# Optimization experiments

Measured on AMD Instinct MI355X. Metric: run time of the kernel, lower is better.

## Reference

```python
import jax, jax.numpy as jnp
import numpy as np

B, S, T = 4096, 2048, 2  # batch of conversations, turns per conversation, num_tags


def setup_inputs() -> dict:
    key = jax.random.key(0)
    k1, k2, k3, k4, k5, k6 = jax.random.split(key, 6)
    emissions = jax.random.normal(k1, (B, S, T), dtype=jnp.float32)
    # learned transition matrices for DistanceCRF branch order:
    # [even2odd, I0, D_consecutive, D_nonconsecutive]
    trans_params = jax.random.normal(k2, (4, T, T), dtype=jnp.float32) * 0.1
    tags = jax.random.randint(k3, (B, S), 0, T)
    who2who = jax.random.randint(k4, (B, S), 0, 2)
    intime = jax.random.randint(k5, (B, S), 0, 3)
    distance = jax.random.randint(k6, (B, S), 0, 4)
    return {"emissions": emissions, "trans_params": trans_params, "tags": tags,
            "who2who": who2who, "intime": intime, "distance": distance}


def _select_trans(trans_params, who2who, intime, distance):
    """Per-step transition matrix selection (DistanceCRF logic).
    Returns [B, S, T, T]."""
    Tn = trans_params.shape[-1]
    # index 0 = zero 'padding' matrix (who2who == -1 case)
    bank = jnp.concatenate([jnp.zeros((1, Tn, Tn), trans_params.dtype), trans_params], axis=0)
    sel = jnp.where(who2who == -1, 0,
          jnp.where(who2who == 1, 1,          # even2odd
          jnp.where(intime == 0, 2,           # I0
          jnp.where(distance == 0, 3, 4))))   # D_consecutive / D_nonconsecutive
    return bank[sel]


def reference(emissions, trans_params, tags, who2who, intime, distance):
    Bn, Sn, Tn = emissions.shape
    trans = _select_trans(trans_params, who2who, intime, distance)  # [B,S,T,T]

    # ---- gold path score ----
    em_gold = jnp.take_along_axis(emissions, tags[..., None], axis=-1)[..., 0].sum(-1)  # [B]
    oh_prev = jax.nn.one_hot(tags[:, :-1], Tn, dtype=emissions.dtype)  # [B,S-1,T]
    oh_cur = jax.nn.one_hot(tags[:, 1:], Tn, dtype=emissions.dtype)
    tr_gold = jnp.einsum('bsij,bsi,bsj->b', trans[:, 1:], oh_prev, oh_cur)  # [B]
    gold_score = em_gold + tr_gold

    # ---- log partition via forward recursion (note: transition added at t=0 too,
    # matching the original implementation) ----
    def step(alpha, xs):
        em_t, tr_t = xs  # [B,T], [B,T,T]
        new_alpha = jax.nn.logsumexp(alpha[:, :, None] + em_t[:, None, :] + tr_t, axis=1)
        return new_alpha, None

    alpha0 = jnp.zeros((Bn, Tn), emissions.dtype)
    xs = (jnp.swapaxes(emissions, 0, 1), jnp.swapaxes(trans, 0, 1))  # [S,B,T], [S,B,T,T]
    alpha, _ = jax.lax.scan(step, alpha0, xs)
    total_score = jax.nn.logsumexp(alpha, axis=-1)  # [B]

    return jnp.stack([gold_score, total_score])  # [2, B]
```

## Files before the change

kernel.cpp:

```cpp
#include <hip/hip_runtime.h>
#include <math.h>

#define Bn 4096
#define Sn 2048
#define BLOCK 256
#define CHUNK (Sn / BLOCK)

__global__ __launch_bounds__(BLOCK, 2) void crf_fwd(
    const float* __restrict__ emissions,
    const float* __restrict__ trans_params,
    const int*   __restrict__ tags,
    const int*   __restrict__ who2who,
    const int*   __restrict__ intime,
    const int*   __restrict__ distance,
    float*       __restrict__ out)
{
    const int b  = blockIdx.x;
    const int t  = threadIdx.x;
    const long base = (long)b * Sn;
    const int s0 = t * CHUNK;

    __shared__ __align__(16) float lbank[20];
    __shared__ __align__(16) float ebank[20];
    __shared__ float wm[4][6];

    const int4* tp = (const int4*)(tags     + base) + t * 2;
    const int4* wp = (const int4*)(who2who  + base) + t * 2;
    const int4* ip = (const int4*)(intime   + base) + t * 2;
    const int4* dp = (const int4*)(distance + base) + t * 2;
    const float4* ep = (const float4*)(emissions + base * 2) + t * 4;

    float4 e0 = ep[0], e1 = ep[1], e2 = ep[2], e3 = ep[3];
    int4 ta = tp[0], tb = tp[1];
    int4 wa = wp[0], wb = wp[1];
    int4 ia = ip[0], ib = ip[1];
    int4 da = dp[0], db = dp[1];
    int prev_tag = (t > 0) ? tags[base + s0 - 1] : 0;

    if (t < 20) {
        float v = (t < 4) ? 0.0f : trans_params[t - 4];
        lbank[t] = v;
        ebank[t] = __expf(v);
    }
    __syncthreads();

    int wv[CHUNK]   = {wa.x, wa.y, wa.z, wa.w, wb.x, wb.y, wb.z, wb.w};
    int iv[CHUNK]   = {ia.x, ia.y, ia.z, ia.w, ib.x, ib.y, ib.z, ib.w};
    int dv[CHUNK]   = {da.x, da.y, da.z, da.w, db.x, db.y, db.z, db.w};
    int tagv[CHUNK] = {ta.x, ta.y, ta.z, ta.w, tb.x, tb.y, tb.z, tb.w};
    float emv[CHUNK][2] = {
        {e0.x, e0.y}, {e0.z, e0.w}, {e1.x, e1.y}, {e1.z, e1.w},
        {e2.x, e2.y}, {e2.z, e2.w}, {e3.x, e3.y}, {e3.z, e3.w}};

    int sel[CHUNK];
    #pragma unroll
    for (int k = 0; k < CHUNK; ++k) {
        int w = wv[k], it = iv[k], d = dv[k];
        sel[k] = (w == -1) ? 0 : (w == 1) ? 1 : (it == 0) ? 2 : (d == 0) ? 3 : 4;
    }
    float4 P[CHUNK];
    #pragma unroll
    for (int k = 0; k < CHUNK; ++k)
        P[k] = *(const float4*)(ebank + sel[k] * 4);

    float x[CHUNK][2];
    #pragma unroll
    for (int k = 0; k < CHUNK; ++k) {
        x[k][0] = __expf(emv[k][0]);
        x[k][1] = __expf(emv[k][1]);
    }

    float m00 = P[0].x * x[0][0], m01 = P[0].y * x[0][1];
    float m10 = P[0].z * x[0][0], m11 = P[0].w * x[0][1];
    float gold = 0.0f;

    #pragma unroll
    for (int k = 1; k < CHUNK; ++k) {
        float n00 = fmaf(m00, P[k].x, m01 * P[k].z) * x[k][0];
        float n01 = fmaf(m00, P[k].y, m01 * P[k].w) * x[k][1];
        float n10 = fmaf(m10, P[k].x, m11 * P[k].z) * x[k][0];
        float n11 = fmaf(m10, P[k].y, m11 * P[k].w) * x[k][1];
        m00 = n00; m01 = n01; m10 = n10; m11 = n11;
    }

    #pragma unroll
    for (int k = 0; k < CHUNK; ++k) {
        int tg = tagv[k];
        gold += tg ? emv[k][1] : emv[k][0];
        if (k > 0 || t > 0) {
            int pt = (k == 0) ? prev_tag : tagv[k - 1];
            gold += lbank[(sel[k] << 2) + (pt << 1) + tg];
        }
    }

    float mx  = fmaxf(fmaxf(m00, m01), fmaxf(m10, m11));
    float inv = 1.0f / mx;
    float L   = __logf(mx);
    m00 *= inv; m01 *= inv; m10 *= inv; m11 *= inv;

    #pragma unroll
    for (int m = 1; m < 64; m <<= 1) {
        float o00 = __shfl_xor(m00, m);
        float o01 = __shfl_xor(m01, m);
        float o10 = __shfl_xor(m10, m);
        float o11 = __shfl_xor(m11, m);
        float oL  = __shfl_xor(L, m);
        float og  = __shfl_xor(gold, m);
        bool up = (t & m) != 0;
        float a00 = up ? o00 : m00, a01 = up ? o01 : m01;
        float a10 = up ? o10 : m10, a11 = up ? o11 : m11;
        float b00 = up ? m00 : o00, b01 = up ? m01 : o01;
        float b10 = up ? m10 : o10, b11 = up ? m11 : o11;
        m00 = fmaf(a00, b00, a01 * b10);
        m01 = fmaf(a00, b01, a01 * b11);
        m10 = fmaf(a10, b00, a11 * b10);
        m11 = fmaf(a10, b01, a11 * b11);
        L += oL;
        gold += og;
    }

    int wave = t >> 6;
    if ((t & 63) == 0) {
        wm[wave][0] = m00; wm[wave][1] = m01;
        wm[wave][2] = m10; wm[wave][3] = m11;
        wm[wave][4] = L;   wm[wave][5] = gold;
    }
    __syncthreads();

    if (t == 0) {
        float r00 = wm[0][0], r01 = wm[0][1], r10 = wm[0][2], r11 = wm[0][3];
        float Ls = wm[0][4], g = wm[0][5];
        #pragma unroll
        for (int q = 1; q < 4; ++q) {
            float q00 = wm[q][0], q01 = wm[q][1], q10 = wm[q][2], q11 = wm[q][3];
            float n00 = fmaf(r00, q00, r01 * q10);
            float n01 = fmaf(r00, q01, r01 * q11);
            float n10 = fmaf(r10, q00, r11 * q10);
            float n11 = fmaf(r10, q01, r11 * q11);
            r00 = n00; r01 = n01; r10 = n10; r11 = n11;
            Ls += wm[q][4];
            g  += wm[q][5];
        }
        float tot = Ls + __logf(r00 + r01 + r10 + r11);
        out[b]      = g;
        out[Bn + b] = tot;
    }
}

extern "C" void kernel_launch(void* const* d_in, const int* in_sizes, int n_in,
                              void* d_out, int out_size, void* d_ws, size_t ws_size,
                              hipStream_t stream) {
    const float* emissions    = (const float*)d_in[0];
    const float* trans_params = (const float*)d_in[1];
    const int*   tags         = (const int*)d_in[2];
    const int*   who2who      = (const int*)d_in[3];
    const int*   intime       = (const int*)d_in[4];
    const int*   distance     = (const int*)d_in[5];
    float* out = (float*)d_out;

    crf_fwd<<<dim3(Bn), dim3(BLOCK), 0, stream>>>(
        emissions, trans_params, tags, who2who, intime, distance, out);
}
```

Measured before the change: 200.8 us.

## Split CRF forward into chunk kernel and per-wave reduction kernel

Splits the fused kernel in two. The first kernel computes per-thread chunk matrices and writes them, normalized, to workspace. A second kernel reduces each sequence with one wave, doing a serial fold of 4 chunks per lane and then a shuffle tree that renormalizes at every step, so the block-wide shared-memory barrier and single-thread tail go away. The change also computes exp and loads transitions inside the recurrence loop instead of precomputing arrays, which should lower register pressure. The cost is an extra launch plus a workspace round trip of about 24 MB, and extra log and reciprocal work in the tree.

```diff
diff --git a/kernel.cpp b/kernel.cpp
--- a/kernel.cpp
+++ b/kernel.cpp
@@ -5,42 +5,44 @@
 #define Sn 2048
 #define BLOCK 256
 #define CHUNK (Sn / BLOCK)
+#define NM (Bn * BLOCK)
 
-__global__ __launch_bounds__(BLOCK, 2) void crf_fwd(
+__global__ __launch_bounds__(BLOCK) void crf_chunk(
     const float* __restrict__ emissions,
     const float* __restrict__ trans_params,
     const int*   __restrict__ tags,
     const int*   __restrict__ who2who,
     const int*   __restrict__ intime,
     const int*   __restrict__ distance,
-    float*       __restrict__ out)
+    float2*      __restrict__ wsA,
+    float2*      __restrict__ wsB,
+    float2*      __restrict__ wsC)
 {
-    const int b  = blockIdx.x;
-    const int t  = threadIdx.x;
+    const int b = blockIdx.x;
+    const int c = threadIdx.x;
     const long base = (long)b * Sn;
-    const int s0 = t * CHUNK;
+    const int s0 = c * CHUNK;
 
     __shared__ __align__(16) float lbank[20];
     __shared__ __align__(16) float ebank[20];
-    __shared__ float wm[4][6];
 
-    const int4* tp = (const int4*)(tags     + base) + t * 2;
-    const int4* wp = (const int4*)(who2who  + base) + t * 2;
-    const int4* ip = (const int4*)(intime   + base) + t * 2;
-    const int4* dp = (const int4*)(distance + base) + t * 2;
-    const float4* ep = (const float4*)(emissions + base * 2) + t * 4;
+    const int4* tp = (const int4*)(tags     + base) + c * 2;
+    const int4* wp = (const int4*)(who2who  + base) + c * 2;
+    const int4* ip = (const int4*)(intime   + base) + c * 2;
+    const int4* dp = (const int4*)(distance + base) + c * 2;
+    const float4* ep = (const float4*)(emissions + base * 2) + c * 4;
 
     float4 e0 = ep[0], e1 = ep[1], e2 = ep[2], e3 = ep[3];
     int4 ta = tp[0], tb = tp[1];
     int4 wa = wp[0], wb = wp[1];
     int4 ia = ip[0], ib = ip[1];
     int4 da = dp[0], db = dp[1];
-    int prev_tag = (t > 0) ? tags[base + s0 - 1] : 0;
+    int prev_tag = (c > 0) ? tags[base + s0 - 1] : 0;
 
-    if (t < 20) {
-        float v = (t < 4) ? 0.0f : trans_params[t - 4];
-        lbank[t] = v;
-        ebank[t] = __expf(v);
+    if (c < 20) {
+        float v = (c < 4) ? 0.0f : trans_params[c - 4];
+        lbank[c] = v;
+        ebank[c] = __expf(v);
     }
     __syncthreads();
 
@@ -58,36 +60,27 @@
         int w = wv[k], it = iv[k], d = dv[k];
         sel[k] = (w == -1) ? 0 : (w == 1) ? 1 : (it == 0) ? 2 : (d == 0) ? 3 : 4;
     }
-    float4 P[CHUNK];
-    #pragma unroll
-    for (int k = 0; k < CHUNK; ++k)
-        P[k] = *(const float4*)(ebank + sel[k] * 4);
 
-    float x[CHUNK][2];
-    #pragma unroll
-    for (int k = 0; k < CHUNK; ++k) {
-        x[k][0] = __expf(emv[k][0]);
-        x[k][1] = __expf(emv[k][1]);
-    }
-
-    float m00 = P[0].x * x[0][0], m01 = P[0].y * x[0][1];
-    float m10 = P[0].z * x[0][0], m11 = P[0].w * x[0][1];
-    float gold = 0.0f;
-
+    float4 P0 = *(const float4*)(ebank + sel[0] * 4);
+    float m00 = P0.x * __expf(emv[0][0]), m01 = P0.y * __expf(emv[0][1]);
+    float m10 = P0.z * __expf(emv[0][0]), m11 = P0.w * __expf(emv[0][1]);
     #pragma unroll
     for (int k = 1; k < CHUNK; ++k) {
-        float n00 = fmaf(m00, P[k].x, m01 * P[k].z) * x[k][0];
-        float n01 = fmaf(m00, P[k].y, m01 * P[k].w) * x[k][1];
-        float n10 = fmaf(m10, P[k].x, m11 * P[k].z) * x[k][0];
-        float n11 = fmaf(m10, P[k].y, m11 * P[k].w) * x[k][1];
+        float4 P = *(const float4*)(ebank + sel[k] * 4);
+        float x0 = __expf(emv[k][0]), x1 = __expf(emv[k][1]);
+        float n00 = fmaf(m00, P.x, m01 * P.z) * x0;
+        float n01 = fmaf(m00, P.y, m01 * P.w) * x1;
+        float n10 = fmaf(m10, P.x, m11 * P.z) * x0;
+        float n11 = fmaf(m10, P.y, m11 * P.w) * x1;
         m00 = n00; m01 = n01; m10 = n10; m11 = n11;
     }
 
+    float gold = 0.0f;
     #pragma unroll
     for (int k = 0; k < CHUNK; ++k) {
         int tg = tagv[k];
         gold += tg ? emv[k][1] : emv[k][0];
-        if (k > 0 || t > 0) {
+        if (k > 0 || c > 0) {
             int pt = (k == 0) ? prev_tag : tagv[k - 1];
             gold += lbank[(sel[k] << 2) + (pt << 1) + tg];
         }
@@ -96,7 +89,54 @@
     float mx  = fmaxf(fmaxf(m00, m01), fmaxf(m10, m11));
     float inv = 1.0f / mx;
     float L   = __logf(mx);
-    m00 *= inv; m01 *= inv; m10 *= inv; m11 *= inv;
+
+    const int gid = b * BLOCK + c;
+    wsA[gid] = make_float2(m00 * inv, m01 * inv);
+    wsB[gid] = make_float2(m10 * inv, m11 * inv);
+    wsC[gid] = make_float2(L, gold);
+}
+
+__global__ __launch_bounds__(BLOCK) void crf_reduce(
+    const float2* __restrict__ wsA,
+    const float2* __restrict__ wsB,
+    const float2* __restrict__ wsC,
+    float*        __restrict__ out)
+{
+    const int lane = threadIdx.x & 63;
+    const int wave = threadIdx.x >> 6;
+    const int b = blockIdx.x * 4 + wave;
+
+    const int idx4 = b * (BLOCK / 2) + lane * 2;
+    const float4* A4 = (const float4*)wsA;
+    const float4* B4 = (const float4*)wsB;
+    const float4* C4 = (const float4*)wsC;
+    float4 a0 = A4[idx4], a1 = A4[idx4 + 1];
+    float4 b0 = B4[idx4], b1 = B4[idx4 + 1];
+    float4 c0 = C4[idx4], c1 = C4[idx4 + 1];
+
+    float m00 = a0.x, m01 = a0.y, m10 = b0.x, m11 = b0.y;
+    float L = c0.x, gold = c0.y;
+    {
+        float q00[3] = {a0.z, a1.x, a1.z};
+        float q01[3] = {a0.w, a1.y, a1.w};
+        float q10[3] = {b0.z, b1.x, b1.z};
+        float q11[3] = {b0.w, b1.y, b1.w};
+        float qL[3]  = {c0.z, c1.x, c1.z};
+        float qg[3]  = {c0.w, c1.y, c1.w};
+        #pragma unroll
+        for (int q = 0; q < 3; ++q) {
+            float n00 = fmaf(m00, q00[q], m01 * q10[q]);
+            float n01 = fmaf(m00, q01[q], m01 * q11[q]);
+            float n10 = fmaf(m10, q00[q], m11 * q10[q]);
+            float n11 = fmaf(m10, q01[q], m11 * q11[q]);
+            m00 = n00; m01 = n01; m10 = n10; m11 = n11;
+            L += qL[q]; gold += qg[q];
+        }
+        float mx  = fmaxf(fmaxf(m00, m01), fmaxf(m10, m11));
+        float inv = 1.0f / mx;
+        L += __logf(mx);
+        m00 *= inv; m01 *= inv; m10 *= inv; m11 *= inv;
+    }
 
     #pragma unroll
     for (int m = 1; m < 64; m <<= 1) {
@@ -106,43 +146,26 @@
         float o11 = __shfl_xor(m11, m);
         float oL  = __shfl_xor(L, m);
         float og  = __shfl_xor(gold, m);
-        bool up = (t & m) != 0;
-        float a00 = up ? o00 : m00, a01 = up ? o01 : m01;
-        float a10 = up ? o10 : m10, a11 = up ? o11 : m11;
-        float b00 = up ? m00 : o00, b01 = up ? m01 : o01;
-        float b10 = up ? m10 : o10, b11 = up ? m11 : o11;
-        m00 = fmaf(a00, b00, a01 * b10);
-        m01 = fmaf(a00, b01, a01 * b11);
-        m10 = fmaf(a10, b00, a11 * b10);
-        m11 = fmaf(a10, b01, a11 * b11);
+        bool up = (lane & m) != 0;
+        float x00 = up ? o00 : m00, x01 = up ? o01 : m01;
+        float x10 = up ? o10 : m10, x11 = up ? o11 : m11;
+        float y00 = up ? m00 : o00, y01 = up ? m01 : o01;
+        float y10 = up ? m10 : o10, y11 = up ? m11 : o11;
+        m00 = fmaf(x00, y00, x01 * y10);
+        m01 = fmaf(x00, y01, x01 * y11);
+        m10 = fmaf(x10, y00, x11 * y10);
+        m11 = fmaf(x10, y01, x11 * y11);
         L += oL;
         gold += og;
+        float mx  = fmaxf(fmaxf(m00, m01), fmaxf(m10, m11));
+        float inv = 1.0f / mx;
+        L += __logf(mx);
+        m00 *= inv; m01 *= inv; m10 *= inv; m11 *= inv;
     }
 
-    int wave = t >> 6;
-    if ((t & 63) == 0) {
-        wm[wave][0] = m00; wm[wave][1] = m01;
-        wm[wave][2] = m10; wm[wave][3] = m11;
-        wm[wave][4] = L;   wm[wave][5] = gold;
-    }
-    __syncthreads();
-
-    if (t == 0) {
-        float r00 = wm[0][0], r01 = wm[0][1], r10 = wm[0][2], r11 = wm[0][3];
-        float Ls = wm[0][4], g = wm[0][5];
-        #pragma unroll
-        for (int q = 1; q < 4; ++q) {
-            float q00 = wm[q][0], q01 = wm[q][1], q10 = wm[q][2], q11 = wm[q][3];
-            float n00 = fmaf(r00, q00, r01 * q10);
-            float n01 = fmaf(r00, q01, r01 * q11);
-            float n10 = fmaf(r10, q00, r11 * q10);
-            float n11 = fmaf(r10, q01, r11 * q11);
-            r00 = n00; r01 = n01; r10 = n10; r11 = n11;
-            Ls += wm[q][4];
-            g  += wm[q][5];
-        }
-        float tot = Ls + __logf(r00 + r01 + r10 + r11);
-        out[b]      = g;
+    if (lane == 0) {
+        float tot = L + __logf(m00 + m01 + m10 + m11);
+        out[b]      = gold;
         out[Bn + b] = tot;
     }
 }
@@ -158,6 +181,13 @@
     const int*   distance     = (const int*)d_in[5];
     float* out = (float*)d_out;
 
-    crf_fwd<<<dim3(Bn), dim3(BLOCK), 0, stream>>>(
-        emissions, trans_params, tags, who2who, intime, distance, out);
+    float2* wsA = (float2*)d_ws;
+    float2* wsB = wsA + NM;
+    float2* wsC = wsB + NM;
+
+    crf_chunk<<<dim3(Bn), dim3(BLOCK), 0, stream>>>(
+        emissions, trans_params, tags, who2who, intime, distance,
+        wsA, wsB, wsC);
+    crf_reduce<<<dim3(Bn / 4), dim3(BLOCK), 0, stream>>>(
+        wsA, wsB, wsC, out);
 }
```

After: 213.0 us. 6.1% more time.
